# Kernel tuning notes

Measured on AMD Instinct MI355X. Metric: run time of the kernel, lower is better.

The kernel has to match this reference:

```python
import jax, jax.numpy as jnp
import numpy as np

BATCH, D_INNER, DT_RANK, N = 256, 5120, 160, 16

def _softplus_thresh(z, threshold=20.0):
    # softplus(z) with beta=1; linear above threshold (matches ttnn.softplus(parameter1=1, parameter2=20))
    return jnp.where(z > threshold, z, jax.nn.softplus(z))

def setup_inputs() -> dict:
    key = jax.random.key(0)
    ks = jax.random.split(key, 9)
    s = lambda d: 1.0 / np.sqrt(d)
    return {
        "x": jax.random.normal(ks[0], (1, 1, BATCH, D_INNER), jnp.float32),
        "h": jax.random.normal(ks[1], (BATCH, D_INNER, N), jnp.float32) * 0.1,
        "W_delta": jax.random.normal(ks[2], (D_INNER, DT_RANK), jnp.float32) * s(D_INNER),
        "W_dt": jax.random.normal(ks[3], (DT_RANK, D_INNER), jnp.float32) * s(DT_RANK),
        "b_dt": jax.random.normal(ks[4], (D_INNER,), jnp.float32) * 0.1,
        "A_log": jax.random.uniform(ks[5], (D_INNER, N), jnp.float32, 0.0, 1.5),
        "W_B": jax.random.normal(ks[6], (D_INNER, N), jnp.float32) * s(D_INNER),
        "W_C": jax.random.normal(ks[7], (D_INNER, N), jnp.float32) * s(D_INNER),
        "D": jax.random.normal(ks[8], (D_INNER,), jnp.float32),
    }

def reference(x, h, W_delta, W_dt, b_dt, A_log, W_B, W_C, D):
    # x: (1,1,B,d_inner) single decode step; h: (B,d_inner,n) SSM state
    xb = x.reshape(BATCH, D_INNER)                           # (B, d)
    # delta = softplus(x @ W_delta @ W_dt + b_dt)           -> (B, d)
    dt = _softplus_thresh((xb @ W_delta) @ W_dt + b_dt)
    A = -jnp.exp(A_log)                                      # (d, n)
    abar = jnp.exp(dt[:, :, None] * A[None, :, :])           # (B, d, n)
    Bp = xb @ W_B                                            # (B, n)
    # bbar * x: delta * B * x, broadcast over state dim
    bx = (dt * xb)[:, :, None] * Bp[:, None, :]              # (B, d, n)
    h_new = abar * h + bx                                    # (B, d, n) new hidden state
    C = xb @ W_C                                             # (B, n)
    y = jnp.einsum("bdn,bn->bd", h_new, C) + xb * D          # readout + skip (D)
    return y.reshape(1, 1, BATCH, D_INNER)
```

## Files before the change

### kernel.cpp

```cpp
#include <hip/hip_runtime.h>
#include <math.h>

#define BATCH 256
#define DIN   5120
#define RANK  160
#define NS    16
#define NCAT  192
#define NSPLIT 40

__global__ __launch_bounds__(256) void k1a_gemm(
    const float* __restrict__ x, const float* __restrict__ Wd,
    const float* __restrict__ WB, const float* __restrict__ WC,
    float* __restrict__ psum)
{
    __shared__ float xT[32][64];
    __shared__ float Wt[32][64];
    const int t  = threadIdx.x;
    const int m0 = blockIdx.x * 64;
    const int n0 = blockIdx.y * 64;
    const int z  = blockIdx.z;
    const int k0 = z * 128;
    const int tm = (t >> 4) * 4;
    const int tn = (t & 15) * 4;

    const int lm  = t >> 2;
    const int lk  = (t & 3) * 8;
    const int ln  = t & 63;
    const int lkb = (t >> 6) * 8;

    const float* wsrc; int wstr;
    {
        const int c = n0 + ln;
        if (c < RANK)            { wsrc = Wd + c;                wstr = RANK; }
        else if (c < RANK + NS)  { wsrc = WB + (c - RANK);       wstr = NS;   }
        else                     { wsrc = WC + (c - RANK - NS);  wstr = NS;   }
    }

    float acc[4][4] = {{0.f}};

    for (int ks = 0; ks < 4; ++ks) {
        const int kb = k0 + ks * 32;
        {
            const float* src = x + (size_t)(m0 + lm) * DIN + kb + lk;
            const float4 a0 = *(const float4*)src;
            const float4 a1 = *(const float4*)(src + 4);
            xT[lk+0][lm]=a0.x; xT[lk+1][lm]=a0.y; xT[lk+2][lm]=a0.z; xT[lk+3][lm]=a0.w;
            xT[lk+4][lm]=a1.x; xT[lk+5][lm]=a1.y; xT[lk+6][lm]=a1.z; xT[lk+7][lm]=a1.w;
        }
        {
            const float* wp = wsrc + (size_t)(kb + lkb) * wstr;
            #pragma unroll
            for (int i = 0; i < 8; ++i) { Wt[lkb + i][ln] = *wp; wp += wstr; }
        }
        __syncthreads();
        #pragma unroll
        for (int k = 0; k < 32; ++k) {
            const float4 a = *(const float4*)&xT[k][tm];
            const float4 b = *(const float4*)&Wt[k][tn];
            acc[0][0] += a.x*b.x; acc[0][1] += a.x*b.y; acc[0][2] += a.x*b.z; acc[0][3] += a.x*b.w;
            acc[1][0] += a.y*b.x; acc[1][1] += a.y*b.y; acc[1][2] += a.y*b.z; acc[1][3] += a.y*b.w;
            acc[2][0] += a.z*b.x; acc[2][1] += a.z*b.y; acc[2][2] += a.z*b.z; acc[2][3] += a.z*b.w;
            acc[3][0] += a.w*b.x; acc[3][1] += a.w*b.y; acc[3][2] += a.w*b.z; acc[3][3] += a.w*b.w;
        }
        __syncthreads();
    }

    float* dst = psum + (size_t)z * (BATCH * NCAT);
    #pragma unroll
    for (int i = 0; i < 4; ++i) {
        const int gm = m0 + tm + i;
        float4 o; o.x = acc[i][0]; o.y = acc[i][1]; o.z = acc[i][2]; o.w = acc[i][3];
        *(float4*)&dst[(size_t)gm * NCAT + n0 + tn] = o;
    }
}

__global__ __launch_bounds__(256) void k1r_reduce(
    const float* __restrict__ psum, const float* __restrict__ A_log,
    float* __restrict__ P, float* __restrict__ Bp, float* __restrict__ Cc,
    float* __restrict__ A2t)
{
    const int g = blockIdx.x * 256 + threadIdx.x;
    A2t[g] = -1.442695041f * __expf(A_log[g]);

    if (blockIdx.x < NCAT) {
        const int o = blockIdx.x * 256 + threadIdx.x;
        float s = 0.f;
        #pragma unroll 8
        for (int z = 0; z < NSPLIT; ++z) s += psum[(size_t)z * (BATCH * NCAT) + o];
        const int gm = o / NCAT;
        const int gc = o - gm * NCAT;
        if (gc < RANK)           P [gm * RANK + gc]             = s;
        else if (gc < RANK + NS) Bp[gm * NS   + gc - RANK]      = s;
        else                     Cc[gm * NS   + gc - RANK - NS] = s;
    }
}

__device__ __forceinline__ float softplus20(float z)
{
    if (z > 20.f) return z;
    return fmaxf(z, 0.f) + log1pf(__expf(-fabsf(z)));
}

__global__ __launch_bounds__(256) void k23_ssm(
    const float* __restrict__ P, const float* __restrict__ Wdt,
    const float* __restrict__ bdt, const float* __restrict__ x,
    const float* __restrict__ h, const float* __restrict__ A2t,
    const float* __restrict__ Bp, const float* __restrict__ Cc,
    const float* __restrict__ Dv, float* __restrict__ y)
{
    __shared__ float aT[32][64];
    __shared__ float Bt[32][64];
    __shared__ float sdt[64][64];

    const int t  = threadIdx.x;
    const int c0 = blockIdx.x * 64;
    const int b0 = blockIdx.y * 64;

    {
        const int tm = (t >> 4) * 4;
        const int tn = (t & 15) * 4;
        const int lm  = t >> 2;
        const int lk  = (t & 3) * 8;
        const int ln  = t & 63;
        const int lkb = (t >> 6) * 8;

        float acc[4][4] = {{0.f}};

        for (int ks = 0; ks < 5; ++ks) {
            const int kb = ks * 32;
            {
                const float* src = P + (size_t)(b0 + lm) * RANK + kb + lk;
                const float4 a0 = *(const float4*)src;
                const float4 a1 = *(const float4*)(src + 4);
                aT[lk+0][lm]=a0.x; aT[lk+1][lm]=a0.y; aT[lk+2][lm]=a0.z; aT[lk+3][lm]=a0.w;
                aT[lk+4][lm]=a1.x; aT[lk+5][lm]=a1.y; aT[lk+6][lm]=a1.z; aT[lk+7][lm]=a1.w;
            }
            {
                const float* wp = Wdt + (size_t)(kb + lkb) * DIN + c0 + ln;
                #pragma unroll
                for (int i = 0; i < 8; ++i) { Bt[lkb + i][ln] = wp[(size_t)i * DIN]; }
            }
            __syncthreads();
            #pragma unroll
            for (int k = 0; k < 32; ++k) {
                const float4 a = *(const float4*)&aT[k][tm];
                const float4 b = *(const float4*)&Bt[k][tn];
                acc[0][0] += a.x*b.x; acc[0][1] += a.x*b.y; acc[0][2] += a.x*b.z; acc[0][3] += a.x*b.w;
                acc[1][0] += a.y*b.x; acc[1][1] += a.y*b.y; acc[1][2] += a.y*b.z; acc[1][3] += a.y*b.w;
                acc[2][0] += a.z*b.x; acc[2][1] += a.z*b.y; acc[2][2] += a.z*b.z; acc[2][3] += a.z*b.w;
                acc[3][0] += a.w*b.x; acc[3][1] += a.w*b.y; acc[3][2] += a.w*b.z; acc[3][3] += a.w*b.w;
            }
            __syncthreads();
        }

        const float4 bz = *(const float4*)&bdt[c0 + tn];
        #pragma unroll
        for (int i = 0; i < 4; ++i) {
            float4 o;
            o.x = softplus20(acc[i][0] + bz.x);
            o.y = softplus20(acc[i][1] + bz.y);
            o.z = softplus20(acc[i][2] + bz.z);
            o.w = softplus20(acc[i][3] + bz.w);
            *(float4*)&sdt[tm + i][tn] = o;
        }
    }
    __syncthreads();

    const int lane = t & 63;
    const int wv   = t >> 6;
    const int v    = lane & 3;
    const int j    = lane >> 2;

    float4 A2q[4]; float dvq[4];
    #pragma unroll
    for (int q = 0; q < 4; ++q) {
        const int c = c0 + q * 16 + j;
        A2q[q] = *(const float4*)(A2t + (size_t)c * NS + v * 4);
        dvq[q] = Dv[c];
    }

    #pragma unroll 4
    for (int bi = 0; bi < 16; ++bi) {
        const int bl = wv * 16 + bi;
        const int gb = b0 + bl;
        const float4 B4 = *(const float4*)(Bp + gb * NS + v * 4);
        const float4 C4 = *(const float4*)(Cc + gb * NS + v * 4);
        float res[4];
        #pragma unroll
        for (int q = 0; q < 4; ++q) {
            const int c = c0 + q * 16 + j;
            const float dtv = sdt[bl][q * 16 + j];
            const float xv  = x[(size_t)gb * DIN + c];
            const float dtx = dtv * xv;
            const float4 h4 = *(const float4*)(h + ((size_t)gb * DIN + c) * NS + v * 4);
            float s;
            s  = (exp2f(dtv * A2q[q].x) * h4.x + dtx * B4.x) * C4.x;
            s += (exp2f(dtv * A2q[q].y) * h4.y + dtx * B4.y) * C4.y;
            s += (exp2f(dtv * A2q[q].z) * h4.z + dtx * B4.z) * C4.z;
            s += (exp2f(dtv * A2q[q].w) * h4.w + dtx * B4.w) * C4.w;
            if (v == 0) s += xv * dvq[q];
            res[q] = s;
        }
        #pragma unroll
        for (int q = 0; q < 4; ++q) {
            res[q] += __shfl_xor(res[q], 1, 64);
            res[q] += __shfl_xor(res[q], 2, 64);
        }
        if (v == 0) {
            #pragma unroll
            for (int q = 0; q < 4; ++q)
                y[(size_t)gb * DIN + c0 + q * 16 + j] = res[q];
        }
    }
}

extern "C" void kernel_launch(void* const* d_in, const int* in_sizes, int n_in,
                              void* d_out, int out_size, void* d_ws, size_t ws_size,
                              hipStream_t stream)
{
    const float* x     = (const float*)d_in[0];
    const float* h     = (const float*)d_in[1];
    const float* Wd    = (const float*)d_in[2];
    const float* Wdt   = (const float*)d_in[3];
    const float* bdt   = (const float*)d_in[4];
    const float* A_log = (const float*)d_in[5];
    const float* WB    = (const float*)d_in[6];
    const float* WC    = (const float*)d_in[7];
    const float* Dv    = (const float*)d_in[8];
    float* out = (float*)d_out;

    float* psum = (float*)d_ws;
    float* P    = psum + (size_t)NSPLIT * BATCH * NCAT;
    float* Bp   = P  + BATCH * RANK;
    float* Cc   = Bp + BATCH * NS;
    float* A2t  = Cc + BATCH * NS;

    k1a_gemm  <<<dim3(4, 3, NSPLIT), 256, 0, stream>>>(x, Wd, WB, WC, psum);
    k1r_reduce<<<dim3(320),          256, 0, stream>>>(psum, A_log, P, Bp, Cc, A2t);
    k23_ssm   <<<dim3(80, 4),        256, 0, stream>>>(P, Wdt, bdt, x, h, A2t, Bp, Cc, Dv, out);
}
```

Before: 181.3 us.

## Split fused dt-GEMM and SSM kernel into two kernels with finer SSM grid

Splits the fused dt-projection GEMM and SSM update into two kernels: k2_dt writes softplus(dt) to a global workspace that reuses the psum buffer, and k3_ssm reads it back. The SSM kernel grid grows from 320 to 1280 blocks, each wave handling 4 batch rows instead of 16, so more parallelism is available to stream the large h tensor. The output store is also spread across all lanes rather than only v==0. In exchange it adds an extra launch and a global round trip of the dt matrix (about 5 MB), and the dt-GEMM stays at 320 blocks.

```diff
diff --git a/kernel.cpp b/kernel.cpp
--- a/kernel.cpp
+++ b/kernel.cpp
@@ -101,73 +101,76 @@
     return fmaxf(z, 0.f) + log1pf(__expf(-fabsf(z)));
 }
 
-__global__ __launch_bounds__(256) void k23_ssm(
+__global__ __launch_bounds__(256) void k2_dt(
     const float* __restrict__ P, const float* __restrict__ Wdt,
-    const float* __restrict__ bdt, const float* __restrict__ x,
+    const float* __restrict__ bdt, float* __restrict__ dtw)
+{
+    __shared__ float aT[32][64];
+    __shared__ float Bt[32][64];
+
+    const int t  = threadIdx.x;
+    const int c0 = blockIdx.x * 64;
+    const int b0 = blockIdx.y * 64;
+
+    const int tm = (t >> 4) * 4;
+    const int tn = (t & 15) * 4;
+    const int lm  = t >> 2;
+    const int lk  = (t & 3) * 8;
+    const int ln  = t & 63;
+    const int lkb = (t >> 6) * 8;
+
+    float acc[4][4] = {{0.f}};
+
+    for (int ks = 0; ks < 5; ++ks) {
+        const int kb = ks * 32;
+        {
+            const float* src = P + (size_t)(b0 + lm) * RANK + kb + lk;
+            const float4 a0 = *(const float4*)src;
+            const float4 a1 = *(const float4*)(src + 4);
+            aT[lk+0][lm]=a0.x; aT[lk+1][lm]=a0.y; aT[lk+2][lm]=a0.z; aT[lk+3][lm]=a0.w;
+            aT[lk+4][lm]=a1.x; aT[lk+5][lm]=a1.y; aT[lk+6][lm]=a1.z; aT[lk+7][lm]=a1.w;
+        }
+        {
+            const float* wp = Wdt + (size_t)(kb + lkb) * DIN + c0 + ln;
+            #pragma unroll
+            for (int i = 0; i < 8; ++i) { Bt[lkb + i][ln] = wp[(size_t)i * DIN]; }
+        }
+        __syncthreads();
+        #pragma unroll
+        for (int k = 0; k < 32; ++k) {
+            const float4 a = *(const float4*)&aT[k][tm];
+            const float4 b = *(const float4*)&Bt[k][tn];
+            acc[0][0] += a.x*b.x; acc[0][1] += a.x*b.y; acc[0][2] += a.x*b.z; acc[0][3] += a.x*b.w;
+            acc[1][0] += a.y*b.x; acc[1][1] += a.y*b.y; acc[1][2] += a.y*b.z; acc[1][3] += a.y*b.w;
+            acc[2][0] += a.z*b.x; acc[2][1] += a.z*b.y; acc[2][2] += a.z*b.z; acc[2][3] += a.z*b.w;
+            acc[3][0] += a.w*b.x; acc[3][1] += a.w*b.y; acc[3][2] += a.w*b.z; acc[3][3] += a.w*b.w;
+        }
+        __syncthreads();
+    }
+
+    const float4 bz = *(const float4*)&bdt[c0 + tn];
+    #pragma unroll
+    for (int i = 0; i < 4; ++i) {
+        float4 o;
+        o.x = softplus20(acc[i][0] + bz.x);
+        o.y = softplus20(acc[i][1] + bz.y);
+        o.z = softplus20(acc[i][2] + bz.z);
+        o.w = softplus20(acc[i][3] + bz.w);
+        *(float4*)&dtw[(size_t)(b0 + tm + i) * DIN + c0 + tn] = o;
+    }
+}
+
+__global__ __launch_bounds__(256) void k3_ssm(
+    const float* __restrict__ dtw, const float* __restrict__ x,
     const float* __restrict__ h, const float* __restrict__ A2t,
     const float* __restrict__ Bp, const float* __restrict__ Cc,
     const float* __restrict__ Dv, float* __restrict__ y)
 {
-    __shared__ float aT[32][64];
-    __shared__ float Bt[32][64];
-    __shared__ float sdt[64][64];
-
-    const int t  = threadIdx.x;
-    const int c0 = blockIdx.x * 64;
-    const int b0 = blockIdx.y * 64;
-
-    {
-        const int tm = (t >> 4) * 4;
-        const int tn = (t & 15) * 4;
-        const int lm  = t >> 2;
-        const int lk  = (t & 3) * 8;
-        const int ln  = t & 63;
-        const int lkb = (t >> 6) * 8;
-
-        float acc[4][4] = {{0.f}};
-
-        for (int ks = 0; ks < 5; ++ks) {
-            const int kb = ks * 32;
-            {
-                const float* src = P + (size_t)(b0 + lm) * RANK + kb + lk;
-                const float4 a0 = *(const float4*)src;
-                const float4 a1 = *(const float4*)(src + 4);
-                aT[lk+0][lm]=a0.x; aT[lk+1][lm]=a0.y; aT[lk+2][lm]=a0.z; aT[lk+3][lm]=a0.w;
-                aT[lk+4][lm]=a1.x; aT[lk+5][lm]=a1.y; aT[lk+6][lm]=a1.z; aT[lk+7][lm]=a1.w;
-            }
-            {
-                const float* wp = Wdt + (size_t)(kb + lkb) * DIN + c0 + ln;
-                #pragma unroll
-                for (int i = 0; i < 8; ++i) { Bt[lkb + i][ln] = wp[(size_t)i * DIN]; }
-            }
-            __syncthreads();
-            #pragma unroll
-            for (int k = 0; k < 32; ++k) {
-                const float4 a = *(const float4*)&aT[k][tm];
-                const float4 b = *(const float4*)&Bt[k][tn];
-                acc[0][0] += a.x*b.x; acc[0][1] += a.x*b.y; acc[0][2] += a.x*b.z; acc[0][3] += a.x*b.w;
-                acc[1][0] += a.y*b.x; acc[1][1] += a.y*b.y; acc[1][2] += a.y*b.z; acc[1][3] += a.y*b.w;
-                acc[2][0] += a.z*b.x; acc[2][1] += a.z*b.y; acc[2][2] += a.z*b.z; acc[2][3] += a.z*b.w;
-                acc[3][0] += a.w*b.x; acc[3][1] += a.w*b.y; acc[3][2] += a.w*b.z; acc[3][3] += a.w*b.w;
-            }
-            __syncthreads();
-        }
-
-        const float4 bz = *(const float4*)&bdt[c0 + tn];
-        #pragma unroll
-        for (int i = 0; i < 4; ++i) {
-            float4 o;
-            o.x = softplus20(acc[i][0] + bz.x);
-            o.y = softplus20(acc[i][1] + bz.y);
-            o.z = softplus20(acc[i][2] + bz.z);
-            o.w = softplus20(acc[i][3] + bz.w);
-            *(float4*)&sdt[tm + i][tn] = o;
-        }
-    }
-    __syncthreads();
-
+    const int t    = threadIdx.x;
     const int lane = t & 63;
     const int wv   = t >> 6;
+    const int c0   = blockIdx.x * 64;
+    const int b0   = (blockIdx.y * 4 + wv) * 4;
     const int v    = lane & 3;
     const int j    = lane >> 2;
 
@@ -179,17 +182,16 @@
         dvq[q] = Dv[c];
     }
 
-    #pragma unroll 4
-    for (int bi = 0; bi < 16; ++bi) {
-        const int bl = wv * 16 + bi;
-        const int gb = b0 + bl;
+    #pragma unroll
+    for (int bi = 0; bi < 4; ++bi) {
+        const int gb = b0 + bi;
         const float4 B4 = *(const float4*)(Bp + gb * NS + v * 4);
         const float4 C4 = *(const float4*)(Cc + gb * NS + v * 4);
         float res[4];
         #pragma unroll
         for (int q = 0; q < 4; ++q) {
             const int c = c0 + q * 16 + j;
-            const float dtv = sdt[bl][q * 16 + j];
+            const float dtv = dtw[(size_t)gb * DIN + c];
             const float xv  = x[(size_t)gb * DIN + c];
             const float dtx = dtv * xv;
             const float4 h4 = *(const float4*)(h + ((size_t)gb * DIN + c) * NS + v * 4);
@@ -206,11 +208,9 @@
             res[q] += __shfl_xor(res[q], 1, 64);
             res[q] += __shfl_xor(res[q], 2, 64);
         }
-        if (v == 0) {
-            #pragma unroll
-            for (int q = 0; q < 4; ++q)
-                y[(size_t)gb * DIN + c0 + q * 16 + j] = res[q];
-        }
+        const float out = (v == 0) ? res[0] : (v == 1) ? res[1]
+                        : (v == 2) ? res[2] : res[3];
+        y[(size_t)gb * DIN + c0 + v * 16 + j] = out;
     }
 }
 
@@ -230,6 +230,7 @@
     float* out = (float*)d_out;
 
     float* psum = (float*)d_ws;
+    float* dtw  = psum;
     float* P    = psum + (size_t)NSPLIT * BATCH * NCAT;
     float* Bp   = P  + BATCH * RANK;
     float* Cc   = Bp + BATCH * NS;
@@ -237,5 +238,6 @@
 
     k1a_gemm  <<<dim3(4, 3, NSPLIT), 256, 0, stream>>>(x, Wd, WB, WC, psum);
     k1r_reduce<<<dim3(320),          256, 0, stream>>>(psum, A_log, P, Bp, Cc, A2t);
-    k23_ssm   <<<dim3(80, 4),        256, 0, stream>>>(P, Wdt, bdt, x, h, A2t, Bp, Cc, Dv, out);
-}
+    k2_dt     <<<dim3(80, 4),        256, 0, stream>>>(P, Wdt, bdt, dtw);
+    k3_ssm    <<<dim3(80, 16),       256, 0, stream>>>(dtw, x, h, A2t, Bp, Cc, Dv, out);
+}
```

Measured after the change: 182.3 us. Within noise of the previous version (+0.5%).
